# Optimization experiments

Hardware: AMD Instinct MI355X
Metric: run time of the kernel (lower is better)

Reference implementation:

```python
import jax, jax.numpy as jnp
import numpy as np

D_MODEL, N_HEAD, D_HEAD = 1024, 16, 64
B, QLEN, MLEN = 4, 1024, 1024
KLEN = QLEN + MLEN  # == rlen
NEG_INF = -1e30


def _rel_shift(x):
    # x: [b, q, rlen, n] -> Transformer-XL relative shift along axis 2
    b, q, rl, n = x.shape
    zero_pad = jnp.zeros((b, q, 1, n), dtype=x.dtype)
    x_padded = jnp.concatenate([zero_pad, x], axis=2)          # [b, q, rl+1, n]
    x_padded = x_padded.reshape(b, rl + 1, q, n)
    return x_padded[:, 1:].reshape(b, q, rl, n)


def setup_inputs() -> dict:
    key = jax.random.key(0)
    ks = jax.random.split(key, 8)
    s = 1.0 / np.sqrt(D_MODEL)
    w = jax.random.normal(ks[0], (B, KLEN, D_MODEL), jnp.float32)
    r = jax.random.normal(ks[1], (1, KLEN, D_MODEL), jnp.float32)
    Wq = jax.random.normal(ks[2], (D_MODEL, N_HEAD * D_HEAD), jnp.float32) * s
    Wkv = jax.random.normal(ks[3], (D_MODEL, 2 * N_HEAD * D_HEAD), jnp.float32) * s
    Wr = jax.random.normal(ks[4], (D_MODEL, N_HEAD * D_HEAD), jnp.float32) * s
    Wo = jax.random.normal(ks[5], (N_HEAD * D_HEAD, D_MODEL), jnp.float32) * s
    bias_w = jax.random.normal(ks[6], (N_HEAD, D_HEAD), jnp.float32) * 0.02
    bias_r = jax.random.normal(ks[7], (N_HEAD, D_HEAD), jnp.float32) * 0.02
    # causal-with-memory mask: query i attends to keys j <= i + MLEN
    i = jnp.arange(QLEN)[:, None]
    j = jnp.arange(KLEN)[None, :]
    attn_mask = j > (i + MLEN)  # True => masked
    return {"w": w, "r": r, "Wq": Wq, "Wkv": Wkv, "Wr": Wr, "Wo": Wo,
            "bias_w": bias_w, "bias_r": bias_r, "attn_mask": attn_mask,
            "qlen": QLEN}


def reference(w, r, Wq, Wkv, Wr, Wo, bias_w, bias_r, attn_mask, qlen):
    bsz, klen, _ = w.shape
    rlen = r.shape[1]
    scale = 1.0 / np.sqrt(D_HEAD)

    q = (w[:, -qlen:] @ Wq).reshape(bsz, qlen, N_HEAD, D_HEAD)
    kv = w @ Wkv
    k, v = jnp.split(kv, 2, axis=-1)
    k = k.reshape(bsz, klen, N_HEAD, D_HEAD)
    v = v.reshape(bsz, klen, N_HEAD, D_HEAD)
    rk = (r @ Wr).reshape(rlen, N_HEAD, D_HEAD)

    AC = jnp.einsum('bind,bjnd->bijn', q + bias_w, k)
    BD = jnp.einsum('bind,jnd->bijn', q + bias_r, rk)
    score = (AC + _rel_shift(BD)) * scale
    score = jnp.where(attn_mask[None, :, :, None], NEG_INF, score)
    prob = jax.nn.softmax(score, axis=2)
    attn_vec = jnp.einsum('bijn,bjnd->bind', prob, v)
    attn_vec = attn_vec.reshape(bsz, qlen, N_HEAD * D_HEAD)
    return attn_vec @ Wo
```

## Files before the change

### kernel.cpp

```cpp
#include <hip/hip_runtime.h>
#include <hip/hip_bf16.h>
#include <stdint.h>


#define DEVI static __device__ __forceinline__

typedef __attribute__((ext_vector_type(8))) short  s8v;
typedef __attribute__((ext_vector_type(4))) float  f4v;
typedef __attribute__((ext_vector_type(2))) int    i2v;
typedef __attribute__((ext_vector_type(4))) float  fl4;

DEVI unsigned short f2b(float f) {
  __hip_bfloat16 h = __float2bfloat16(f);
  return __builtin_bit_cast(unsigned short, h);
}

DEVI f4v MFMA(s8v a, s8v b, f4v c) {
  return __builtin_amdgcn_mfma_f32_16x16x32_bf16(a, b, c, 0, 0, 0);
}

DEVI void gl_lds16(const void* g, void* lds) {
  __builtin_amdgcn_global_load_lds(
      (const __attribute__((address_space(1))) unsigned int*)g,
      (__attribute__((address_space(3))) unsigned int*)lds, 16, 0, 0);
}

__global__ void transpose_all(const float* __restrict__ Wq,
                              const float* __restrict__ Wkv,
                              const float* __restrict__ Wr,
                              const float* __restrict__ Wo,
                              unsigned short* __restrict__ WqT,
                              unsigned short* __restrict__ WkvT,
                              unsigned short* __restrict__ WrT,
                              unsigned short* __restrict__ WoT) {
  __shared__ float tile[32][33];
  const int bx = blockIdx.x;
  const float* W;
  unsigned short* WT;
  int N, nb;
  if (bx < 32)       { W = Wq;  WT = WqT;  N = 1024; nb = bx; }
  else if (bx < 96)  { W = Wkv; WT = WkvT; N = 2048; nb = bx - 32; }
  else if (bx < 128) { W = Wr;  WT = WrT;  N = 1024; nb = bx - 96; }
  else               { W = Wo;  WT = WoT;  N = 1024; nb = bx - 128; }
  int n0 = nb * 32, k0 = blockIdx.y * 32;
  int tx = threadIdx.x, ty = threadIdx.y;
#pragma unroll
  for (int i = 0; i < 4; ++i)
    tile[ty + i * 8][tx] = W[(size_t)(k0 + ty + i * 8) * N + n0 + tx];
  __syncthreads();
#pragma unroll
  for (int i = 0; i < 4; ++i)
    WT[(size_t)(n0 + ty + i * 8) * 1024 + k0 + tx] = f2b(tile[tx][ty + i * 8]);
}

__global__ void transpose_v(const unsigned short* __restrict__ in,
                            unsigned short* __restrict__ out) {
  __shared__ unsigned short Ts[64 * 72];
  const int t = threadIdx.x;
  const int j0 = blockIdx.x * 64;
  const size_t bh = blockIdx.y;
#pragma unroll
  for (int p = 0; p < 2; ++p) {
    int cc = t + p * 256;
    int j = cc >> 3, d0 = (cc & 7) * 8;
    s8v v = *(const s8v*)(in + (bh * 2048 + j0 + j) * 64 + d0);
    *(s8v*)(Ts + j * 72 + d0) = v;
  }
  __syncthreads();
  const int d = t >> 2, jc = (t & 3) * 16;
  s8v a, b;
#pragma unroll
  for (int e = 0; e < 8; ++e) a[e] = (short)Ts[(jc + e) * 72 + d];
#pragma unroll
  for (int e = 0; e < 8; ++e) b[e] = (short)Ts[(jc + 8 + e) * 72 + d];
  *(s8v*)(out + (bh * 64 + d) * 2048 + j0 + jc) = a;
  *(s8v*)(out + (bh * 64 + d) * 2048 + j0 + jc + 8) = b;
}

template <int MODE>
__global__ __launch_bounds__(256, 2) void gemm_kern(
    const float* __restrict__ A, const unsigned short* __restrict__ A16,
    const unsigned short* __restrict__ BT, unsigned short* __restrict__ O1,
    unsigned short* __restrict__ O2, float* __restrict__ Of,
    const float* __restrict__ biasw, const float* __restrict__ biasr) {
  __shared__ unsigned short As[2][128 * 32];
  __shared__ unsigned short Bs[2][128 * 32];
  const int t = threadIdx.x, l = t & 63, w = t >> 6;
  const int g = l >> 4, lr = l & 15;
  const int bm = blockIdx.x, bn = blockIdx.y;
  const int wr = w >> 1, wc = w & 1;
  const float QSC = 0.18033688f;
  f4v acc[4][4] = {};

  auto stageB = [&](int k0, int buf) {
#pragma unroll
    for (int ss = 0; ss < 2; ++ss) {
      int idx = w * 64 + ss * 256 + l;
      int row = idx >> 2, c = idx & 3;
      gl_lds16(BT + (size_t)(bn * 128 + row) * 1024 + k0 + c * 8,
               (void*)(Bs[buf] + (w * 64 + ss * 256) * 8));
    }
  };
  auto stageA_lds = [&](int k0, int buf) {
#pragma unroll
    for (int ss = 0; ss < 2; ++ss) {
      int idx = w * 64 + ss * 256 + l;
      int row = idx >> 2, c = idx & 3;
      gl_lds16(A16 + (size_t)(bm * 128 + row) * 1024 + k0 + c * 8,
               (void*)(As[buf] + (w * 64 + ss * 256) * 8));
    }
  };
  auto loadA = [&](int k0, fl4* regs) {
#pragma unroll
    for (int ss = 0; ss < 4; ++ss) {
      int idx = t + ss * 256;
      int row = idx >> 3, c = idx & 7;
      int grow = bm * 128 + row;
      size_t arow = (MODE == 0)
                        ? ((size_t)(grow >> 10) * 2048 + 1024 + (grow & 1023))
                        : (size_t)grow;
      regs[ss] = *(const fl4*)(A + arow * 1024 + k0 + c * 4);
    }
  };
  auto writeA = [&](const fl4* regs, int buf) {
#pragma unroll
    for (int ss = 0; ss < 4; ++ss) {
      int idx = t + ss * 256;
      int row = idx >> 3, c = idx & 7;
      fl4 v = regs[ss];
      unsigned int p0 = f2b(v.x) | ((unsigned int)f2b(v.y) << 16);
      unsigned int p1 = f2b(v.z) | ((unsigned int)f2b(v.w) << 16);
      i2v pv; pv.x = (int)p0; pv.y = (int)p1;
      *(i2v*)(As[buf] + row * 32 + c * 4) = pv;
    }
  };

  stageB(0, 0);
  if (MODE == 3) {
    stageA_lds(0, 0);
  } else {
    fl4 r0[4];
    loadA(0, r0);
    writeA(r0, 0);
  }
  __syncthreads();

  int cur = 0;
  for (int step = 0; step < 32; ++step) {
    const bool nx = step < 31;
    const int nk0 = (step + 1) * 32;
    fl4 aregs[4];
    if (nx) {
      stageB(nk0, cur ^ 1);
      if (MODE == 3) stageA_lds(nk0, cur ^ 1);
      else loadA(nk0, aregs);
    }
    s8v af[4], bf[4];
#pragma unroll
    for (int m = 0; m < 4; ++m)
      af[m] = *(const s8v*)(As[cur] + (wr * 64 + m * 16 + lr) * 32 + g * 8);
#pragma unroll
    for (int n = 0; n < 4; ++n)
      bf[n] = *(const s8v*)(Bs[cur] + (wc * 64 + n * 16 + lr) * 32 + g * 8);
#pragma unroll
    for (int m = 0; m < 4; ++m)
#pragma unroll
      for (int n = 0; n < 4; ++n) acc[m][n] = MFMA(af[m], bf[n], acc[m][n]);
    if (nx && MODE != 3) writeA(aregs, cur ^ 1);
    __syncthreads();
    cur ^= 1;
  }

#pragma unroll
  for (int m = 0; m < 4; ++m) {
#pragma unroll
    for (int n = 0; n < 4; ++n) {
#pragma unroll
      for (int r = 0; r < 4; ++r) {
        int row = bm * 128 + wr * 64 + m * 16 + g * 4 + r;
        int col = bn * 128 + wc * 64 + n * 16 + lr;
        float v = acc[m][n][r];
        if (MODE == 0) {
          int b = row >> 10, i = row & 1023;
          int nh = col >> 6, d = col & 63;
          size_t o = ((size_t)(b * 16 + nh) * 1024 + i) * 64 + d;
          O1[o] = f2b((v + biasw[col]) * QSC);
          O2[o] = f2b((v + biasr[col]) * QSC);
        } else if (MODE == 1) {
          int b = row >> 11, j = row & 2047;
          if (col < 1024)
            O1[((size_t)(b * 16 + (col >> 6)) * 2048 + j) * 64 + (col & 63)] =
                f2b(v);
          else
            O2[((size_t)(b * 16 + ((col - 1024) >> 6)) * 2048 + j) * 64 +
               (col & 63)] = f2b(v);
        } else if (MODE == 2) {
          O1[((size_t)(col >> 6) * 2048 + row) * 64 + (col & 63)] = f2b(v);
        } else {
          Of[(size_t)row * 1024 + col] = v;
        }
      }
    }
  }
}

__global__ __launch_bounds__(256, 2) void attn_kern(
    const unsigned short* __restrict__ qw, const unsigned short* __restrict__ qr,
    const unsigned short* __restrict__ kk, const unsigned short* __restrict__ vt,
    const unsigned short* __restrict__ rkp, unsigned short* __restrict__ av) {
  __shared__ unsigned short Ks[64 * 64];
  __shared__ unsigned short Vs[64 * 64];
  __shared__ unsigned short Rs[128 * 64];
  __shared__ unsigned short Pn[4][1024];
  const int t = threadIdx.x, l = t & 63, w = t >> 6;
  const int g = l >> 4, lr = l & 15;
  const int i0 = ((blockIdx.x * 5) & 15) * 64;
  const int n = blockIdx.y, b = blockIdx.z;
  const size_t bn = (size_t)(b * 16 + n);
  const unsigned short* qwb = qw + bn * 1024 * 64;
  const unsigned short* qrb = qr + bn * 1024 * 64;
  const unsigned short* kb = kk + bn * 2048 * 64;
  const unsigned short* vb = vt + bn * 64 * 2048;
  const unsigned short* rb = rkp + (size_t)n * 2048 * 64;

  const int qi = i0 + w * 16 + lr;
  s8v aqw[2], aqr[2];
#pragma unroll
  for (int ks = 0; ks < 2; ++ks) {
    aqw[ks] = *(const s8v*)(qwb + (size_t)qi * 64 + ks * 32 + g * 8);
    aqr[ks] = *(const s8v*)(qrb + (size_t)qi * 64 + ks * 32 + g * 8);
  }

  s8v ONES;
#pragma unroll
  for (int e = 0; e < 8; ++e) ONES[e] = (short)0x3F80;

  f4v acco[4] = {};
  f4v accl = {};
  float mrow[4] = {-3e38f, -3e38f, -3e38f, -3e38f};

  const int ntile = (i0 + 1088) >> 6;

  auto stage = [&](int jt) {
    const int j0 = jt * 64;
    const int m0 = j0 + 960 - i0;
#pragma unroll
    for (int ss = 0; ss < 2; ++ss) {
      int idx = w * 64 + ss * 256 + l;
      int row = idx >> 3, c = idx & 7;
      gl_lds16(kb + (size_t)(j0 + row) * 64 + ((c ^ (row & 7)) * 8),
               (void*)(Ks + (w * 64 + ss * 256) * 8));
    }
#pragma unroll
    for (int ss = 0; ss < 2; ++ss) {
      int idx = w * 64 + ss * 256 + l;
      int d = idx >> 3, c = idx & 7;
      gl_lds16(vb + (size_t)d * 2048 + j0 + ((c ^ (d & 7)) * 8),
               (void*)(Vs + (w * 64 + ss * 256) * 8));
    }
#pragma unroll
    for (int ss = 0; ss < 4; ++ss) {
      int idx = w * 64 + ss * 256 + l;
      int rr = idx >> 3, c = idx & 7;
      int m = m0 + rr;
      if (m > 2047) m = 2047;
      gl_lds16(rb + (size_t)m * 64 + ((c ^ (rr & 7)) * 8),
               (void*)(Rs + (w * 64 + ss * 256) * 8));
    }
  };

  for (int jt = 0; jt < ntile; ++jt) {
    const int j0 = jt * 64;
    stage(jt);
    __syncthreads();
    const bool mt = (jt == ntile - 1);

    f4v accs[4] = {};
    f4v acce[5] = {};
#pragma unroll
    for (int ks = 0; ks < 2; ++ks) {
#pragma unroll
      for (int jf = 0; jf < 4; ++jf) {
        int row = jf * 16 + lr;
        s8v bk =
            *(const s8v*)(Ks + row * 64 + (((ks * 4 + g) ^ (row & 7)) * 8));
        accs[jf] = MFMA(aqw[ks], bk, accs[jf]);
      }
#pragma unroll
      for (int ef = 0; ef < 5; ++ef) {
        int row = (3 - w + ef) * 16 + lr;
        s8v br =
            *(const s8v*)(Rs + row * 64 + (((ks * 4 + g) ^ (row & 7)) * 8));
        acce[ef] = MFMA(aqr[ks], br, acce[ef]);
      }
    }

    float P[4][4];
#pragma unroll
    for (int r = 0; r < 4; ++r) {
      const int s = 15 - 4 * g - r;
      const int src = (l & 48) | ((lr + s) & 15);
      const int carry = (lr + s) >> 4;
      float es[5];
#pragma unroll
      for (int f = 0; f < 5; ++f) es[f] = __shfl(acce[f][r], src, 64);
      float pmax = -3e38f;
#pragma unroll
      for (int jf = 0; jf < 4; ++jf) {
        float sv = accs[jf][r] + (carry ? es[jf + 1] : es[jf]);
        if (mt) {
          int jg = j0 + jf * 16 + lr;
          int ig = i0 + w * 16 + 4 * g + r;
          if (jg > ig + 1024) sv = -3e38f;
        }
        P[jf][r] = sv;
        pmax = fmaxf(pmax, sv);
      }
      if (!__all(pmax <= mrow[r] + 8.0f)) {
        float rmax = pmax;
#pragma unroll
        for (int dd = 1; dd < 16; dd <<= 1)
          rmax = fmaxf(rmax, __shfl_xor(rmax, dd, 64));
        float nm = fmaxf(mrow[r], rmax);
        float corr = exp2f(mrow[r] - nm);
        mrow[r] = nm;
#pragma unroll
        for (int df = 0; df < 4; ++df) acco[df][r] *= corr;
        accl[r] *= corr;
      }
#pragma unroll
      for (int jf = 0; jf < 4; ++jf) P[jf][r] = exp2f(P[jf][r] - mrow[r]);
    }

#pragma unroll
    for (int jf = 0; jf < 4; ++jf) {
#pragma unroll
      for (int r = 0; r < 4; ++r) {
        int ip = 4 * g + r;
        int cj = (jf * 2 + (lr >> 3)) ^ (ip & 7);
        Pn[w][ip * 64 + cj * 8 + (lr & 7)] = f2b(P[jf][r]);
      }
    }
    asm volatile("s_waitcnt lgkmcnt(0)" ::: "memory");
    __builtin_amdgcn_sched_barrier(0);

#pragma unroll
    for (int ks = 0; ks < 2; ++ks) {
      s8v ap =
          *(const s8v*)(Pn[w] + lr * 64 + (((ks * 4 + g) ^ (lr & 7)) * 8));
      accl = MFMA(ap, ONES, accl);
#pragma unroll
      for (int df = 0; df < 4; ++df) {
        int vrow = df * 16 + lr;
        s8v bv = *(const s8v*)(Vs + vrow * 64 +
                               (((ks * 4 + g) ^ (vrow & 7)) * 8));
        acco[df] = MFMA(ap, bv, acco[df]);
      }
    }
    __syncthreads();
  }

#pragma unroll
  for (int r = 0; r < 4; ++r) {
    float inv = 1.0f / accl[r];
    int ig = i0 + w * 16 + 4 * g + r;
#pragma unroll
    for (int df = 0; df < 4; ++df)
      av[((size_t)b * 1024 + ig) * 1024 + n * 64 + df * 16 + lr] =
          f2b(acco[df][r] * inv);
  }
}

extern "C" void kernel_launch(void* const* d_in, const int* in_sizes, int n_in,
                              void* d_out, int out_size, void* d_ws,
                              size_t ws_size, hipStream_t stream) {
  (void)in_sizes; (void)n_in; (void)out_size; (void)ws_size;
  const float* w   = (const float*)d_in[0];
  const float* r   = (const float*)d_in[1];
  const float* Wq  = (const float*)d_in[2];
  const float* Wkv = (const float*)d_in[3];
  const float* Wr  = (const float*)d_in[4];
  const float* Wo  = (const float*)d_in[5];
  const float* bw  = (const float*)d_in[6];
  const float* br  = (const float*)d_in[7];

  char* ws = (char*)d_ws;
  const size_t MB = 1024 * 1024;
  unsigned short* WqT  = (unsigned short*)(ws + 0 * MB);
  unsigned short* WkvT = (unsigned short*)(ws + 2 * MB);
  unsigned short* WrT  = (unsigned short*)(ws + 6 * MB);
  unsigned short* WoT  = (unsigned short*)(ws + 8 * MB);
  unsigned short* qwb  = (unsigned short*)(ws + 10 * MB);
  unsigned short* qrb  = (unsigned short*)(ws + 18 * MB);
  unsigned short* kbf  = (unsigned short*)(ws + 26 * MB);
  unsigned short* vbf  = (unsigned short*)(ws + 42 * MB);
  unsigned short* rkb  = (unsigned short*)(ws + 58 * MB);
  unsigned short* avb  = (unsigned short*)(ws + 62 * MB);
  unsigned short* vtb  = (unsigned short*)d_out;

  hipLaunchKernelGGL(transpose_all, dim3(160, 32), dim3(32, 8), 0, stream,
                     Wq, Wkv, Wr, Wo, WqT, WkvT, WrT, WoT);

  hipLaunchKernelGGL((gemm_kern<0>), dim3(32, 8), dim3(256), 0, stream,
                     w, (const unsigned short*)nullptr, WqT, qwb, qrb,
                     (float*)nullptr, bw, br);
  hipLaunchKernelGGL((gemm_kern<1>), dim3(64, 16), dim3(256), 0, stream,
                     w, (const unsigned short*)nullptr, WkvT, kbf, vbf,
                     (float*)nullptr, (const float*)nullptr,
                     (const float*)nullptr);
  hipLaunchKernelGGL((gemm_kern<2>), dim3(16, 8), dim3(256), 0, stream,
                     r, (const unsigned short*)nullptr, WrT, rkb,
                     (unsigned short*)nullptr, (float*)nullptr,
                     (const float*)nullptr, (const float*)nullptr);

  hipLaunchKernelGGL(transpose_v, dim3(32, 64), dim3(256), 0, stream, vbf, vtb);

  hipLaunchKernelGGL(attn_kern, dim3(16, 16, 4), dim3(256), 0, stream,
                     qwb, qrb, kbf, vtb, rkb, avb);

  hipLaunchKernelGGL((gemm_kern<3>), dim3(32, 8), dim3(256), 0, stream,
                     (const float*)nullptr, avb, WoT, (unsigned short*)nullptr,
                     (unsigned short*)nullptr, (float*)d_out,
                     (const float*)nullptr, (const float*)nullptr);
}
```

Measured before the change: 495.3 us.

## Pair mirrored query tiles per attention block to balance causal work and share K/V

Each attention block now processes two query tiles, i0 and 960-i0, whose causal tile counts sum to a constant. The two tiles share each staged K/V tile, and each keeps its own relative-position buffer and P scratch. The grid is halved, so blocks have equal work and K/V global loads are halved. The cost is more registers and LDS per block (two accumulator sets, extra R and P buffers), which may lower occupancy under launch_bounds(256,2). The grid also drops to 512 blocks.

```diff
diff --git a/kernel.cpp b/kernel.cpp
--- a/kernel.cpp
+++ b/kernel.cpp
@@ -210,11 +210,15 @@
     const unsigned short* __restrict__ rkp, unsigned short* __restrict__ av) {
   __shared__ unsigned short Ks[64 * 64];
   __shared__ unsigned short Vs[64 * 64];
-  __shared__ unsigned short Rs[128 * 64];
-  __shared__ unsigned short Pn[4][1024];
+  __shared__ unsigned short Ra[128 * 64];
+  __shared__ unsigned short Rb[128 * 64];
+  __shared__ unsigned short Pa[4][1024];
+  __shared__ unsigned short Pb[4][1024];
   const int t = threadIdx.x, l = t & 63, w = t >> 6;
   const int g = l >> 4, lr = l & 15;
-  const int i0 = ((blockIdx.x * 5) & 15) * 64;
+  const int bx = blockIdx.x;
+  const int i0a = bx * 64, i0b = 960 - i0a;
+  const int nta = bx + 17, ntb = 32 - bx;
   const int n = blockIdx.y, b = blockIdx.z;
   const size_t bn = (size_t)(b * 16 + n);
   const unsigned short* qwb = qw + bn * 1024 * 64;
@@ -223,41 +227,27 @@
   const unsigned short* vb = vt + bn * 64 * 2048;
   const unsigned short* rb = rkp + (size_t)n * 2048 * 64;
 
-  const int qi = i0 + w * 16 + lr;
-  s8v aqw[2], aqr[2];
+  const int qia = i0a + w * 16 + lr;
+  const int qib = i0b + w * 16 + lr;
+  s8v aqw_a[2], aqr_a[2], aqw_b[2], aqr_b[2];
 #pragma unroll
   for (int ks = 0; ks < 2; ++ks) {
-    aqw[ks] = *(const s8v*)(qwb + (size_t)qi * 64 + ks * 32 + g * 8);
-    aqr[ks] = *(const s8v*)(qrb + (size_t)qi * 64 + ks * 32 + g * 8);
+    aqw_a[ks] = *(const s8v*)(qwb + (size_t)qia * 64 + ks * 32 + g * 8);
+    aqr_a[ks] = *(const s8v*)(qrb + (size_t)qia * 64 + ks * 32 + g * 8);
+    aqw_b[ks] = *(const s8v*)(qwb + (size_t)qib * 64 + ks * 32 + g * 8);
+    aqr_b[ks] = *(const s8v*)(qrb + (size_t)qib * 64 + ks * 32 + g * 8);
   }
 
   s8v ONES;
 #pragma unroll
   for (int e = 0; e < 8; ++e) ONES[e] = (short)0x3F80;
 
-  f4v acco[4] = {};
-  f4v accl = {};
-  float mrow[4] = {-3e38f, -3e38f, -3e38f, -3e38f};
-
-  const int ntile = (i0 + 1088) >> 6;
-
-  auto stage = [&](int jt) {
-    const int j0 = jt * 64;
-    const int m0 = j0 + 960 - i0;
-#pragma unroll
-    for (int ss = 0; ss < 2; ++ss) {
-      int idx = w * 64 + ss * 256 + l;
-      int row = idx >> 3, c = idx & 7;
-      gl_lds16(kb + (size_t)(j0 + row) * 64 + ((c ^ (row & 7)) * 8),
-               (void*)(Ks + (w * 64 + ss * 256) * 8));
-    }
-#pragma unroll
-    for (int ss = 0; ss < 2; ++ss) {
-      int idx = w * 64 + ss * 256 + l;
-      int d = idx >> 3, c = idx & 7;
-      gl_lds16(vb + (size_t)d * 2048 + j0 + ((c ^ (d & 7)) * 8),
-               (void*)(Vs + (w * 64 + ss * 256) * 8));
-    }
+  f4v acco_a[4] = {}, acco_b[4] = {};
+  f4v accl_a = {}, accl_b = {};
+  float mrow_a[4] = {-3e38f, -3e38f, -3e38f, -3e38f};
+  float mrow_b[4] = {-3e38f, -3e38f, -3e38f, -3e38f};
+
+  auto stageR = [&](unsigned short* Rx, int m0) {
 #pragma unroll
     for (int ss = 0; ss < 4; ++ss) {
       int idx = w * 64 + ss * 256 + l;
@@ -265,16 +255,33 @@
       int m = m0 + rr;
       if (m > 2047) m = 2047;
       gl_lds16(rb + (size_t)m * 64 + ((c ^ (rr & 7)) * 8),
-               (void*)(Rs + (w * 64 + ss * 256) * 8));
-    }
-  };
-
-  for (int jt = 0; jt < ntile; ++jt) {
+               (void*)(Rx + (w * 64 + ss * 256) * 8));
+    }
+  };
+
+  auto stage = [&](int jt) {
     const int j0 = jt * 64;
-    stage(jt);
-    __syncthreads();
-    const bool mt = (jt == ntile - 1);
-
+#pragma unroll
+    for (int ss = 0; ss < 2; ++ss) {
+      int idx = w * 64 + ss * 256 + l;
+      int row = idx >> 3, c = idx & 7;
+      gl_lds16(kb + (size_t)(j0 + row) * 64 + ((c ^ (row & 7)) * 8),
+               (void*)(Ks + (w * 64 + ss * 256) * 8));
+    }
+#pragma unroll
+    for (int ss = 0; ss < 2; ++ss) {
+      int idx = w * 64 + ss * 256 + l;
+      int d = idx >> 3, c = idx & 7;
+      gl_lds16(vb + (size_t)d * 2048 + j0 + ((c ^ (d & 7)) * 8),
+               (void*)(Vs + (w * 64 + ss * 256) * 8));
+    }
+    if (jt < nta) stageR(Ra, j0 + 960 - i0a);
+    stageR(Rb, j0 + i0a);
+  };
+
+  auto phase = [&](const unsigned short* Rx, unsigned short* Px,
+                   const s8v* paqw, const s8v* paqr, f4v* acco, f4v& accl,
+                   float* mrow, bool mt, int i0, int j0) {
     f4v accs[4] = {};
     f4v acce[5] = {};
 #pragma unroll
@@ -284,14 +291,14 @@
         int row = jf * 16 + lr;
         s8v bk =
             *(const s8v*)(Ks + row * 64 + (((ks * 4 + g) ^ (row & 7)) * 8));
-        accs[jf] = MFMA(aqw[ks], bk, accs[jf]);
+        accs[jf] = MFMA(paqw[ks], bk, accs[jf]);
       }
 #pragma unroll
       for (int ef = 0; ef < 5; ++ef) {
         int row = (3 - w + ef) * 16 + lr;
         s8v br =
-            *(const s8v*)(Rs + row * 64 + (((ks * 4 + g) ^ (row & 7)) * 8));
-        acce[ef] = MFMA(aqr[ks], br, acce[ef]);
+            *(const s8v*)(Rx + row * 64 + (((ks * 4 + g) ^ (row & 7)) * 8));
+        acce[ef] = MFMA(paqr[ks], br, acce[ef]);
       }
     }
 
@@ -338,7 +345,7 @@
       for (int r = 0; r < 4; ++r) {
         int ip = 4 * g + r;
         int cj = (jf * 2 + (lr >> 3)) ^ (ip & 7);
-        Pn[w][ip * 64 + cj * 8 + (lr & 7)] = f2b(P[jf][r]);
+        Px[ip * 64 + cj * 8 + (lr & 7)] = f2b(P[jf][r]);
       }
     }
     asm volatile("s_waitcnt lgkmcnt(0)" ::: "memory");
@@ -346,8 +353,7 @@
 
 #pragma unroll
     for (int ks = 0; ks < 2; ++ks) {
-      s8v ap =
-          *(const s8v*)(Pn[w] + lr * 64 + (((ks * 4 + g) ^ (lr & 7)) * 8));
+      s8v ap = *(const s8v*)(Px + lr * 64 + (((ks * 4 + g) ^ (lr & 7)) * 8));
       accl = MFMA(ap, ONES, accl);
 #pragma unroll
       for (int df = 0; df < 4; ++df) {
@@ -357,17 +363,33 @@
         acco[df] = MFMA(ap, bv, acco[df]);
       }
     }
+  };
+
+  for (int jt = 0; jt < ntb; ++jt) {
+    const int j0 = jt * 64;
+    stage(jt);
     __syncthreads();
+    if (jt < nta)
+      phase(Ra, Pa[w], aqw_a, aqr_a, acco_a, accl_a, mrow_a,
+            jt == nta - 1, i0a, j0);
+    phase(Rb, Pb[w], aqw_b, aqr_b, acco_b, accl_b, mrow_b,
+          jt == ntb - 1, i0b, j0);
+    __syncthreads();
   }
 
 #pragma unroll
   for (int r = 0; r < 4; ++r) {
-    float inv = 1.0f / accl[r];
-    int ig = i0 + w * 16 + 4 * g + r;
-#pragma unroll
-    for (int df = 0; df < 4; ++df)
-      av[((size_t)b * 1024 + ig) * 1024 + n * 64 + df * 16 + lr] =
-          f2b(acco[df][r] * inv);
+    float inva = 1.0f / accl_a[r];
+    float invb = 1.0f / accl_b[r];
+    int iga = i0a + w * 16 + 4 * g + r;
+    int igb = i0b + w * 16 + 4 * g + r;
+#pragma unroll
+    for (int df = 0; df < 4; ++df) {
+      av[((size_t)b * 1024 + iga) * 1024 + n * 64 + df * 16 + lr] =
+          f2b(acco_a[df][r] * inva);
+      av[((size_t)b * 1024 + igb) * 1024 + n * 64 + df * 16 + lr] =
+          f2b(acco_b[df][r] * invb);
+    }
   }
 }
 
@@ -415,7 +437,7 @@
 
   hipLaunchKernelGGL(transpose_v, dim3(32, 64), dim3(256), 0, stream, vbf, vtb);
 
-  hipLaunchKernelGGL(attn_kern, dim3(16, 16, 4), dim3(256), 0, stream,
+  hipLaunchKernelGGL(attn_kern, dim3(8, 16, 4), dim3(256), 0, stream,
                      qwb, qrb, kbf, vtb, rkb, avb);
 
   hipLaunchKernelGGL((gemm_kern<3>), dim3(32, 8), dim3(256), 0, stream,
```

Measured after the change: 425.2 us. 14.2% less time.
